# Optimization experiments

Measured on AMD Instinct MI355X. Metric: run time of the kernel, lower is better.

The kernel has to match this reference:

```python
import jax, jax.numpy as jnp
import numpy as np

# Model dims (match init_kwargs)
N_P, NV, P, S = 60, 5, 20, 14   # particles, vertices, pf features, sv features
HID, DE, DO, NCLS, BATCH = 60, 20, 24, 2, 512

# Rr/Rs one-hot matrices encode edges (r, s) for r != s with r varying slowest.
# So gather-by-Rr == repeat each node N-1 times, gather-by-Rs == index by senders,
# and scatter-sum by Rr^T == reshape to [B, N, N-1, De] and sum axis 2.
_SENDERS = np.array([s for r in range(N_P) for s in range(N_P) if s != r])


def _lin_params(key, din, dout):
    kw, kb = jax.random.split(key)
    bound = 1.0 / np.sqrt(din)
    w = jax.random.uniform(kw, (din, dout), minval=-bound, maxval=bound, dtype=jnp.float32)
    b = jax.random.uniform(kb, (dout,), minval=-bound, maxval=bound, dtype=jnp.float32)
    return w, b


def setup_inputs() -> dict:
    key = jax.random.key(0)
    ks = jax.random.split(key, 12)
    inp = {
        'x': jax.random.normal(ks[0], (BATCH, P, N_P), dtype=jnp.float32),
        'y': jax.random.normal(ks[1], (BATCH, S, NV), dtype=jnp.float32),
    }
    specs = [('fr', [(2 * P, HID), (HID, HID), (HID, DE)]),
             ('pv', [(S + P, HID), (HID, HID), (HID, DE)]),
             ('fo', [(P + 2 * DE, HID), (HID, HID), (HID, DO)])]
    ki = 2
    for name, dims in specs:
        for j, (di, do) in enumerate(dims, 1):
            w, b = _lin_params(ks[ki], di, do)
            ki += 1
            inp[f'{name}_w{j}'] = w
            inp[f'{name}_b{j}'] = b
    w, b = _lin_params(ks[11], DO, NCLS)
    inp['fc_w'] = w
    inp['fc_b'] = b
    return inp


def _mlp3(h, w1, b1, w2, b2, w3, b3):
    h = jax.nn.relu(h @ w1 + b1)
    h = jax.nn.relu(h @ w2 + b2)
    return jax.nn.relu(h @ w3 + b3)


def reference(x, y, fr_w1, fr_b1, fr_w2, fr_b2, fr_w3, fr_b3,
              pv_w1, pv_b1, pv_w2, pv_b2, pv_w3, pv_b3,
              fo_w1, fo_b1, fo_w2, fo_b2, fo_w3, fo_b3, fc_w, fc_b):
    xt = jnp.swapaxes(x, -1, -2)  # [B, N, P]
    yt = jnp.swapaxes(y, -1, -2)  # [B, Nv, S]
    B = xt.shape[0]

    # particle-particle edge conv (gather via index, scatter-sum via reshape)
    Orr = jnp.repeat(xt, N_P - 1, axis=1)          # [B, Nr, P], receiver features
    Ors = xt[:, _SENDERS]                          # [B, Nr, P], sender features
    E = _mlp3(jnp.concatenate([Orr, Ors], axis=-1),
              fr_w1, fr_b1, fr_w2, fr_b2, fr_w3, fr_b3)  # [B, Nr, De]
    Ebar_pp = E.reshape(B, N_P, N_P - 1, DE).sum(axis=2)  # [B, N, De]

    # particle-vertex edge conv (Rk repeats particles, Rv tiles vertices)
    Ork = jnp.repeat(xt, NV, axis=1)               # [B, Nt, P]
    Orv = jnp.tile(yt, (1, N_P, 1))                # [B, Nt, S]
    E2 = _mlp3(jnp.concatenate([Ork, Orv], axis=-1),
               pv_w1, pv_b1, pv_w2, pv_b2, pv_w3, pv_b3)  # [B, Nt, De]
    Ebar_pv = E2.reshape(B, N_P, NV, DE).sum(axis=2)      # [B, N, De]

    C = jnp.concatenate([xt, Ebar_pp, Ebar_pv], axis=-1)  # [B, N, P + 2*De]
    O = _mlp3(C, fo_w1, fo_b1, fo_w2, fo_b2, fo_w3, fo_b3)  # [B, N, Do]
    return O.sum(axis=-2) @ fc_w + fc_b  # [B, num_classes]
```

## Files before the change

kernel.cpp:

```cpp
#include <hip/hip_runtime.h>

#define BATCH 512
#define NPART 60
#define PFEAT 20
#define SFEAT 14
#define NVTX  5
#define HID   60
#define DE    20
#define DO    24
#define NCLS  2
#define SR    68

typedef _Float16 half8  __attribute__((ext_vector_type(8)));
typedef _Float16 half4v __attribute__((ext_vector_type(4)));
typedef __fp16   fp16x2 __attribute__((ext_vector_type(2)));
typedef float    f32x4  __attribute__((ext_vector_type(4)));

__device__ __forceinline__ half4v pkcvt4(f32x4 a) {
    fp16x2 lo = __builtin_amdgcn_cvt_pkrtz(a[0], a[1]);
    fp16x2 hi = __builtin_amdgcn_cvt_pkrtz(a[2], a[3]);
    half4v r;
    r[0] = (_Float16)lo[0]; r[1] = (_Float16)lo[1];
    r[2] = (_Float16)hi[0]; r[3] = (_Float16)hi[1];
    return r;
}
__device__ __forceinline__ half4v relu4(half4v a) {
#pragma unroll
    for (int j = 0; j < 4; ++j)
        a[j] = (a[j] > (_Float16)0.f) ? a[j] : (_Float16)0.f;
    return a;
}

__global__ __launch_bounds__(256) void prep_kernel(
    const float* __restrict__ x, const float* __restrict__ y,
    const float* __restrict__ fr_w1, const float* __restrict__ fr_b1,
    const float* __restrict__ pv_w1, const float* __restrict__ pv_b1,
    const float* __restrict__ fr_w2, const float* __restrict__ fr_b2,
    const float* __restrict__ fr_w3, const float* __restrict__ fr_b3,
    const float* __restrict__ pv_w2, const float* __restrict__ pv_b2,
    const float* __restrict__ pv_w3, const float* __restrict__ pv_b3,
    const float* __restrict__ fo_w1, const float* __restrict__ fo_b1,
    const float* __restrict__ fo_w2, const float* __restrict__ fo_b2,
    const float* __restrict__ fo_w3, const float* __restrict__ fo_b3,
    _Float16* __restrict__ frW2p, _Float16* __restrict__ frW3p16,
    _Float16* __restrict__ pvW2p, _Float16* __restrict__ pvW3p16,
    _Float16* __restrict__ foW1p, _Float16* __restrict__ foW2p16,
    _Float16* __restrict__ foW3p16,
    _Float16* __restrict__ frW1Ap, _Float16* __restrict__ frW1Bp,
    _Float16* __restrict__ pvW1Ap, _Float16* __restrict__ xp,
    _Float16* __restrict__ pvvp)
{
    if (blockIdx.x < 16) {
        int idx = blockIdx.x*256 + threadIdx.x;
        {
            int j  = idx & 7;
            int L  = (idx >> 3) & 63;
            int kk = (idx >> 9) & 1;
            int u  = idx >> 10;
            int k  = kk*32 + (L >> 4)*8 + j;
            int n  = u*16 + (L & 15);
            float v2f = 0.f, v2p = 0.f, v1o = 0.f;
            if (k < HID && n < HID) {
                v2f = fr_w2[k*HID + n];
                v2p = pv_w2[k*HID + n];
                v1o = fo_w1[k*HID + n];
            } else if (k == HID) {
                if (n < HID)      { v2f = fr_b2[n]; v2p = pv_b2[n]; v1o = fo_b1[n]; }
                else if (n == HID){ v2f = 1.f;      v2p = 1.f;      v1o = 1.f; }
            }
            frW2p[idx] = (_Float16)v2f;
            pvW2p[idx] = (_Float16)v2p;
            foW1p[idx] = (_Float16)v1o;
        }
        {
            int j  = idx & 3;
            int L  = (idx >> 2) & 63;
            int kt = (idx >> 8) & 3;
            int u  = idx >> 10;
            int k  = kt*16 + (L >> 4)*4 + j;
            int n  = u*16 + (L & 15);
            float v = 0.f;
            if (k < HID && n < HID)        v = fo_w2[k*HID + n];
            else if (k == HID) {
                if (n < HID)       v = fo_b2[n];
                else if (n == HID) v = 1.f;
            }
            foW2p16[idx] = (_Float16)v;
        }
        if (idx < 2048) {
            {
                int j  = idx & 3;
                int L  = (idx >> 2) & 63;
                int kt = (idx >> 8) & 3;
                int u  = idx >> 10;
                int k  = kt*16 + (L >> 4)*4 + j;
                int n  = u*16 + (L & 15);
                float vf = 0.f, vp = 0.f, vo = 0.f;
                if (k < HID) {
                    if (n < DE) { vf = fr_w3[k*DE + n]; vp = pv_w3[k*DE + n]; }
                    if (n < DO)   vo = fo_w3[k*DO + n];
                } else if (k == HID) {
                    if (n < DE) { vf = fr_b3[n]; vp = pv_b3[n]; }
                    if (n < DO)   vo = fo_b3[n];
                }
                frW3p16[idx] = (_Float16)vf;
                pvW3p16[idx] = (_Float16)vp;
                foW3p16[idx] = (_Float16)vo;
            }
            {
                int j = idx & 7;
                int L = (idx >> 3) & 63;
                int u = idx >> 9;
                int k = (L >> 4)*8 + j;
                int n = u*16 + (L & 15);
                float va = 0.f, vb = 0.f, vpv = 0.f;
                if (k < PFEAT && n < HID) {
                    va  = fr_w1[k*HID + n];
                    vb  = fr_w1[(PFEAT + k)*HID + n];
                    vpv = pv_w1[k*HID + n];
                } else if (k == PFEAT) {
                    if (n < HID)       va = fr_b1[n];
                    else if (n == HID) va = 1.f;
                }
                frW1Ap[idx] = (_Float16)va;
                frW1Bp[idx] = (_Float16)vb;
                pvW1Ap[idx] = (_Float16)vpv;
            }
        }
    } else if (blockIdx.x < 16 + 480) {
        int idx = (blockIdx.x - 16)*256 + threadIdx.x;
        if (idx < BATCH*NPART*4) {
            int p = idx % NPART;
            int t = idx / NPART;
            int q = t & 3;
            int b = t >> 2;
            half8 v;
#pragma unroll
            for (int j = 0; j < 8; ++j) {
                int k = q*8 + j;
                float f = 0.f;
                if (k < PFEAT)       f = x[((size_t)b*PFEAT + k)*NPART + p];
                else if (k == PFEAT) f = 1.f;
                v[j] = (_Float16)f;
            }
            *(half8*)(xp + (size_t)idx*8) = v;
        }
    } else {
        int idx = (blockIdx.x - (16 + 480))*256 + threadIdx.x;
        if (idx < BATCH*NVTX*64) {
            int h = idx & 63;
            int t = idx >> 6;
            int v = t % NVTX;
            int b = t / NVTX;
            float a;
            if (h < HID) {
                a = pv_b1[h];
#pragma unroll
                for (int f = 0; f < SFEAT; ++f)
                    a += y[((size_t)b*SFEAT + f)*NVTX + v] * pv_w1[(PFEAT + f)*HID + h];
            } else {
                a = (h == HID) ? 1.f : 0.f;
            }
            pvvp[idx] = (_Float16)a;
        }
    }
}

__global__ __launch_bounds__(512) void fused_kernel(
    const float* __restrict__ fcw, const float* __restrict__ fcb,
    const half8*  __restrict__ frw2p, const half4v* __restrict__ frw3p16,
    const half8*  __restrict__ pvw2p, const half4v* __restrict__ pvw3p16,
    const half8*  __restrict__ fow1p, const half4v* __restrict__ fow2p16,
    const half4v* __restrict__ fow3p16,
    const half8*  __restrict__ frw1ap, const half8* __restrict__ frw1bp,
    const half8*  __restrict__ pvw1ap, const _Float16* __restrict__ xp,
    const half8*  __restrict__ pvvp,
    float* __restrict__ out)
{
    __shared__ __align__(16) _Float16 sFrA[NPART*SR];
    __shared__ __align__(16) _Float16 sFrB[NPART*SR];
    __shared__ __align__(16) _Float16 sPvA[NPART*SR];
    __shared__ __align__(16) _Float16 sEpp[NPART*DE];
    __shared__ __align__(16) _Float16 sEpvP[NVTX*NPART*DE];
    __shared__ __align__(16) float    sDsum[4][DO];
    _Float16* sCin = sFrA;

    const f32x4 z4 = {0.f, 0.f, 0.f, 0.f};

    int bb   = blockIdx.x;
    int wv   = threadIdx.x >> 6;
    int lane = threadIdx.x & 63;
    int ml   = lane & 15;
    int q    = lane >> 4;

    half4v onesA;
#pragma unroll
    for (int j = 0; j < 4; ++j) onesA[j] = (_Float16)1.f;

    {
        int tile = wv & 3;
        int row  = 16*tile + ml;
        int rr   = (row < NPART) ? row : 0;
        half8 bX = *(const half8*)(xp + (((size_t)bb*4 + q)*NPART + rr)*8);
#pragma unroll
        for (int task = 0; task < 2; ++task) {
            const half8* Wt; _Float16* Ot;
            if (wv < 4) {
                if (task == 0) { Wt = frw1ap; Ot = sFrA; }
                else           { Wt = pvw1ap; Ot = sPvA; }
            } else {
                if (task == 1) break;
                Wt = frw1bp; Ot = sFrB;
            }
#pragma unroll
            for (int u = 0; u < 4; ++u) {
                half8 w8 = Wt[u*64 + lane];
                f32x4 acc = z4;
                acc = __builtin_amdgcn_mfma_f32_16x16x32_f16(w8, bX, acc, 0, 0, 0);
                if (row < NPART)
                    *(half4v*)(Ot + row*SR + u*16 + 4*q) = pkcvt4(acc);
            }
        }
    }
    __syncthreads();

    {
        half8  w2r[8];
        half4v w3r[8];
#pragma unroll
        for (int t = 0; t < 8; ++t) w2r[t] = frw2p[t*64 + lane];
#pragma unroll
        for (int t = 0; t < 8; ++t) w3r[t] = frw3p16[t*64 + lane];
#pragma unroll
        for (int t = 0; t < 8; ++t) {
            asm volatile("" : "+v"(w2r[t]));
            asm volatile("" : "+v"(w3r[t]));
        }
        half4v m3;
#pragma unroll
        for (int j = 0; j < 4; ++j) m3[j] = (_Float16)((4*q + j < 11) ? 1.f : 0.f);

        for (int r = wv; r < NPART; r += 8) {
            half8 u8k0 = *(const half8*)(sFrA + r*SR + q*8);
            half8 u8k1 = *(const half8*)(sFrA + r*SR + 32 + q*8);
            f32x4 accS0 = z4, accS1 = z4;

#pragma unroll
            for (int c = 0; c < 4; ++c) {
                int edge = 16*c + ml;
                int sr = (edge < NPART-1) ? (edge + (edge >= r)) : 0;
                half8 bA0, bA1;
                {
                    half8 v8 = *(const half8*)(sFrB + sr*SR + q*8);
                    half8 s8 = u8k0 + v8;
#pragma unroll
                    for (int j = 0; j < 8; ++j)
                        s8[j] = (s8[j] > (_Float16)0.f) ? s8[j] : (_Float16)0.f;
                    bA0 = s8;
                    v8 = *(const half8*)(sFrB + sr*SR + 32 + q*8);
                    s8 = u8k1 + v8;
#pragma unroll
                    for (int j = 0; j < 8; ++j)
                        s8[j] = (s8[j] > (_Float16)0.f) ? s8[j] : (_Float16)0.f;
                    bA1 = s8;
                }
                half4v a3u[4];
#pragma unroll
                for (int u = 0; u < 4; ++u) {
                    f32x4 a = z4;
                    a = __builtin_amdgcn_mfma_f32_16x16x32_f16(w2r[u*2 + 0], bA0, a, 0, 0, 0);
                    a = __builtin_amdgcn_mfma_f32_16x16x32_f16(w2r[u*2 + 1], bA1, a, 0, 0, 0);
                    a3u[u] = relu4(pkcvt4(a));
                }
                f32x4 e0 = z4, e1 = z4;
#pragma unroll
                for (int u = 0; u < 4; ++u) {
                    e0 = __builtin_amdgcn_mfma_f32_16x16x16f16(a3u[u], w3r[0*4 + u], e0, 0, 0, 0);
                    e1 = __builtin_amdgcn_mfma_f32_16x16x16f16(a3u[u], w3r[1*4 + u], e1, 0, 0, 0);
                }
                half4v p0 = relu4(pkcvt4(e0));
                half4v p1 = relu4(pkcvt4(e1));
                if (c == 3) { p0 *= m3; p1 *= m3; }
                accS0 = __builtin_amdgcn_mfma_f32_16x16x16f16(onesA, p0, accS0, 0, 0, 0);
                accS1 = __builtin_amdgcn_mfma_f32_16x16x16f16(onesA, p1, accS1, 0, 0, 0);
            }
            if (q == 0) {
                sEpp[r*DE + ml] = (_Float16)accS0[0];
                if (ml < DE - 16)
                    sEpp[r*DE + 16 + ml] = (_Float16)accS1[0];
            }
        }
    }

    if (wv >= 4) {
        half8  w2r[8];
        half4v w3r[8];
#pragma unroll
        for (int t = 0; t < 8; ++t) w2r[t] = pvw2p[t*64 + lane];
#pragma unroll
        for (int t = 0; t < 8; ++t) w3r[t] = pvw3p16[t*64 + lane];
#pragma unroll
        for (int t = 0; t < 8; ++t) {
            asm volatile("" : "+v"(w2r[t]));
            asm volatile("" : "+v"(w3r[t]));
        }
        for (int kunit = wv - 4; kunit < 20; kunit += 4) {
            int gv = kunit >> 2;
            int tl = kunit & 3;
            int p  = 16*tl + ml;
            int sp = (p < NPART) ? p : 0;
            const half8* pvvB = pvvp + ((size_t)bb*NVTX + gv)*8;
            half8 u8k0 = pvvB[q];
            half8 u8k1 = pvvB[4 + q];

            half8 bA[2];
#pragma unroll
            for (int kk = 0; kk < 2; ++kk) {
                half8 v8 = *(const half8*)(sPvA + sp*SR + kk*32 + q*8);
                half8 s8 = (kk ? u8k1 : u8k0) + v8;
#pragma unroll
                for (int j = 0; j < 8; ++j) {
                    _Float16 vj = s8[j];
                    s8[j] = (vj > (_Float16)0.f) ? vj : (_Float16)0.f;
                }
                bA[kk] = s8;
            }
            f32x4 acc3[2];
            acc3[0] = z4; acc3[1] = z4;
#pragma unroll
            for (int u = 0; u < 4; ++u) {
                f32x4 a = z4;
                a = __builtin_amdgcn_mfma_f32_16x16x32_f16(w2r[u*2 + 0], bA[0], a, 0, 0, 0);
                a = __builtin_amdgcn_mfma_f32_16x16x32_f16(w2r[u*2 + 1], bA[1], a, 0, 0, 0);
                half4v a3u = relu4(pkcvt4(a));
                acc3[0] = __builtin_amdgcn_mfma_f32_16x16x16f16(w3r[0*4 + u], a3u, acc3[0], 0, 0, 0);
                acc3[1] = __builtin_amdgcn_mfma_f32_16x16x16f16(w3r[1*4 + u], a3u, acc3[1], 0, 0, 0);
            }
#pragma unroll
            for (int v = 0; v < 2; ++v) {
                int col4 = v*16 + 4*q;
                if (p < NPART && col4 < DE) {
                    half4v hv = relu4(pkcvt4(acc3[v]));
                    *(half4v*)(sEpvP + (gv*NPART + p)*DE + col4) = hv;
                }
            }
        }
    }
    __syncthreads();

    for (int idx = threadIdx.x; idx < NPART*64; idx += 512) {
        int p = idx >> 6;
        int k = idx & 63;
        _Float16 v;
        if (k < PFEAT) {
            v = xp[(((size_t)bb*4 + (k >> 3))*NPART + p)*8 + (k & 7)];
        } else if (k < PFEAT + DE) {
            v = sEpp[p*DE + (k - PFEAT)];
        } else if (k < PFEAT + 2*DE) {
            int c = k - PFEAT - DE;
            float s = 0.f;
#pragma unroll
            for (int g5 = 0; g5 < NVTX; ++g5)
                s += (float)sEpvP[(g5*NPART + p)*DE + c];
            v = (_Float16)s;
        } else {
            v = (k == HID) ? (_Float16)1.f : (_Float16)0.f;
        }
        sCin[p*SR + k] = v;
    }
    __syncthreads();

    if (wv < 4) {
        int p = 16*wv + ml;
        int sp = (p < NPART) ? p : 0;
        half8 bC[2];
#pragma unroll
        for (int kk = 0; kk < 2; ++kk)
            bC[kk] = *(const half8*)(sCin + sp*SR + kk*32 + q*8);

        f32x4 acc1[4];
#pragma unroll
        for (int u = 0; u < 4; ++u) {
            acc1[u] = z4;
            acc1[u] = __builtin_amdgcn_mfma_f32_16x16x32_f16(fow1p[(u*2 + 0)*64 + lane], bC[0], acc1[u], 0, 0, 0);
            acc1[u] = __builtin_amdgcn_mfma_f32_16x16x32_f16(fow1p[(u*2 + 1)*64 + lane], bC[1], acc1[u], 0, 0, 0);
        }
        half4v a2[4];
#pragma unroll
        for (int u = 0; u < 4; ++u) a2[u] = relu4(pkcvt4(acc1[u]));

        f32x4 acc2[4];
#pragma unroll
        for (int u = 0; u < 4; ++u) {
            acc2[u] = z4;
#pragma unroll
            for (int kt = 0; kt < 4; ++kt)
                acc2[u] = __builtin_amdgcn_mfma_f32_16x16x16f16(fow2p16[(u*4 + kt)*64 + lane], a2[kt], acc2[u], 0, 0, 0);
        }
        half4v a3[4];
#pragma unroll
        for (int u = 0; u < 4; ++u) a3[u] = relu4(pkcvt4(acc2[u]));

        f32x4 e0 = z4, e1 = z4;
#pragma unroll
        for (int u = 0; u < 4; ++u) {
            e0 = __builtin_amdgcn_mfma_f32_16x16x16f16(a3[u], fow3p16[(0*4 + u)*64 + lane], e0, 0, 0, 0);
            e1 = __builtin_amdgcn_mfma_f32_16x16x16f16(a3[u], fow3p16[(1*4 + u)*64 + lane], e1, 0, 0, 0);
        }
        half4v p0 = relu4(pkcvt4(e0));
        half4v p1 = relu4(pkcvt4(e1));
        if (wv == 3 && q == 3) {
#pragma unroll
            for (int j = 0; j < 4; ++j) { p0[j] = (_Float16)0.f; p1[j] = (_Float16)0.f; }
        }
        f32x4 accP0 = __builtin_amdgcn_mfma_f32_16x16x16f16(onesA, p0, z4, 0, 0, 0);
        f32x4 accP1 = __builtin_amdgcn_mfma_f32_16x16x16f16(onesA, p1, z4, 0, 0, 0);
        if (q == 0) {
            sDsum[wv][ml] = accP0[0];
            if (ml < DO - 16)
                sDsum[wv][16 + ml] = accP1[0];
        }
    }
    __syncthreads();

    if (wv == 0) {
        float tot = 0.f;
        if (lane < DO) {
#pragma unroll
            for (int w4 = 0; w4 < 4; ++w4) tot += sDsum[w4][lane];
        }
        float p0 = (lane < DO) ? tot * fcw[lane*NCLS + 0] : 0.f;
        float p1 = (lane < DO) ? tot * fcw[lane*NCLS + 1] : 0.f;
#pragma unroll
        for (int d = 1; d <= 16; d <<= 1) {
            p0 += __shfl_xor(p0, d);
            p1 += __shfl_xor(p1, d);
        }
        if (lane == 0) {
            out[bb*NCLS + 0] = p0 + fcb[0];
            out[bb*NCLS + 1] = p1 + fcb[1];
        }
    }
}

extern "C" void kernel_launch(void* const* d_in, const int* in_sizes, int n_in,
                              void* d_out, int out_size, void* d_ws, size_t ws_size,
                              hipStream_t stream)
{
    const float* x     = (const float*)d_in[0];
    const float* y     = (const float*)d_in[1];
    const float* fr_w1 = (const float*)d_in[2];
    const float* fr_b1 = (const float*)d_in[3];
    const float* fr_w2 = (const float*)d_in[4];
    const float* fr_b2 = (const float*)d_in[5];
    const float* fr_w3 = (const float*)d_in[6];
    const float* fr_b3 = (const float*)d_in[7];
    const float* pv_w1 = (const float*)d_in[8];
    const float* pv_b1 = (const float*)d_in[9];
    const float* pv_w2 = (const float*)d_in[10];
    const float* pv_b2 = (const float*)d_in[11];
    const float* pv_w3 = (const float*)d_in[12];
    const float* pv_b3 = (const float*)d_in[13];
    const float* fo_w1 = (const float*)d_in[14];
    const float* fo_b1 = (const float*)d_in[15];
    const float* fo_w2 = (const float*)d_in[16];
    const float* fo_b2 = (const float*)d_in[17];
    const float* fo_w3 = (const float*)d_in[18];
    const float* fo_b3 = (const float*)d_in[19];
    const float* fc_w  = (const float*)d_in[20];
    const float* fc_b  = (const float*)d_in[21];
    float* out = (float*)d_out;

    char* wsb = (char*)d_ws;
    size_t off = 0;
    auto alloc = [&](size_t bytes) { char* p = wsb + off; off += (bytes + 255) & ~(size_t)255; return p; };

    _Float16* frW2p   = (_Float16*)alloc(4096*2);
    _Float16* frW3p16 = (_Float16*)alloc(2048*2);
    _Float16* pvW2p   = (_Float16*)alloc(4096*2);
    _Float16* pvW3p16 = (_Float16*)alloc(2048*2);
    _Float16* foW1p   = (_Float16*)alloc(4096*2);
    _Float16* foW2p16 = (_Float16*)alloc(4096*2);
    _Float16* foW3p16 = (_Float16*)alloc(2048*2);
    _Float16* frW1Ap  = (_Float16*)alloc(2048*2);
    _Float16* frW1Bp  = (_Float16*)alloc(2048*2);
    _Float16* pvW1Ap  = (_Float16*)alloc(2048*2);
    _Float16* xp      = (_Float16*)alloc((size_t)BATCH*NPART*32*2);
    _Float16* pvvp    = (_Float16*)alloc((size_t)BATCH*NVTX*64*2);

    int xblocks  = (BATCH*NPART*4 + 255)/256;
    int pvblocks = (BATCH*NVTX*64 + 255)/256;
    prep_kernel<<<16 + xblocks + pvblocks, 256, 0, stream>>>(
        x, y, fr_w1, fr_b1, pv_w1, pv_b1,
        fr_w2, fr_b2, fr_w3, fr_b3,
        pv_w2, pv_b2, pv_w3, pv_b3,
        fo_w1, fo_b1, fo_w2, fo_b2, fo_w3, fo_b3,
        frW2p, frW3p16, pvW2p, pvW3p16, foW1p, foW2p16, foW3p16,
        frW1Ap, frW1Bp, pvW1Ap, xp, pvvp);

    fused_kernel<<<BATCH, 512, 0, stream>>>(
        fc_w, fc_b,
        (const half8*)frW2p, (const half4v*)frW3p16,
        (const half8*)pvW2p, (const half4v*)pvW3p16,
        (const half8*)foW1p, (const half4v*)foW2p16, (const half4v*)foW3p16,
        (const half8*)frW1Ap, (const half8*)frW1Bp,
        (const half8*)pvW1Ap, xp, (const half8*)pvvp,
        out);
}
```

Before: 134.4 us.

## Use 16x16x32 MFMA for layer 2/3, sentinel padding row, register-accumulate PV edges

Repacks the second- and third-layer weights so the K=64 products run as two 16x16x32 f16 MFMAs instead of four 16x16x16 ones. Adds a sentinel sender row set to a large negative value, so padded edges go through ReLU to zero without a per-tile mask multiply. The particle-vertex path now has each wave own one particle tile, loop over vertices and accumulate the ReLU outputs in registers. This removes the 5x staging buffer in shared memory and the later summation pass. Particle-particle sums are written straight into the C-input buffer, which drops the sEpp copy and reduces LDS use, with the risk that the repacked weight layouts must exactly match the MFMA operand layout.

```diff
diff --git a/kernel.cpp b/kernel.cpp
--- a/kernel.cpp
+++ b/kernel.cpp
@@ -29,6 +29,21 @@
     for (int j = 0; j < 4; ++j)
         a[j] = (a[j] > (_Float16)0.f) ? a[j] : (_Float16)0.f;
     return a;
+}
+__device__ __forceinline__ half8 cvtrelu8(f32x4 a, f32x4 b) {
+    fp16x2 c0 = __builtin_amdgcn_cvt_pkrtz(a[0], a[1]);
+    fp16x2 c1 = __builtin_amdgcn_cvt_pkrtz(a[2], a[3]);
+    fp16x2 c2 = __builtin_amdgcn_cvt_pkrtz(b[0], b[1]);
+    fp16x2 c3 = __builtin_amdgcn_cvt_pkrtz(b[2], b[3]);
+    half8 r;
+    r[0] = (_Float16)c0[0]; r[1] = (_Float16)c0[1];
+    r[2] = (_Float16)c1[0]; r[3] = (_Float16)c1[1];
+    r[4] = (_Float16)c2[0]; r[5] = (_Float16)c2[1];
+    r[6] = (_Float16)c3[0]; r[7] = (_Float16)c3[1];
+#pragma unroll
+    for (int j = 0; j < 8; ++j)
+        r[j] = (r[j] > (_Float16)0.f) ? r[j] : (_Float16)0.f;
+    return r;
 }
 
 __global__ __launch_bounds__(256) void prep_kernel(
@@ -42,10 +57,10 @@
     const float* __restrict__ fo_w1, const float* __restrict__ fo_b1,
     const float* __restrict__ fo_w2, const float* __restrict__ fo_b2,
     const float* __restrict__ fo_w3, const float* __restrict__ fo_b3,
-    _Float16* __restrict__ frW2p, _Float16* __restrict__ frW3p16,
-    _Float16* __restrict__ pvW2p, _Float16* __restrict__ pvW3p16,
-    _Float16* __restrict__ foW1p, _Float16* __restrict__ foW2p16,
-    _Float16* __restrict__ foW3p16,
+    _Float16* __restrict__ frW2p, _Float16* __restrict__ frW3x,
+    _Float16* __restrict__ pvW2p, _Float16* __restrict__ pvW3x,
+    _Float16* __restrict__ foW1p, _Float16* __restrict__ foW2x,
+    _Float16* __restrict__ foW3x,
     _Float16* __restrict__ frW1Ap, _Float16* __restrict__ frW1Bp,
     _Float16* __restrict__ pvW1Ap, _Float16* __restrict__ xp,
     _Float16* __restrict__ pvvp)
@@ -73,28 +88,30 @@
             foW1p[idx] = (_Float16)v1o;
         }
         {
-            int j  = idx & 3;
-            int L  = (idx >> 2) & 63;
-            int kt = (idx >> 8) & 3;
-            int u  = idx >> 10;
-            int k  = kt*16 + (L >> 4)*4 + j;
-            int n  = u*16 + (L & 15);
+            int j    = idx & 7;
+            int L    = (idx >> 3) & 63;
+            int pair = (idx >> 9) & 1;
+            int u    = idx >> 10;
+            int qq   = L >> 4;
+            int k    = pair*32 + ((j < 4) ? (qq*4 + j) : (16 + qq*4 + (j - 4)));
+            int n    = u*16 + (L & 15);
             float v = 0.f;
-            if (k < HID && n < HID)        v = fo_w2[k*HID + n];
+            if (k < HID) { if (n < HID) v = fo_w2[k*HID + n]; }
             else if (k == HID) {
                 if (n < HID)       v = fo_b2[n];
                 else if (n == HID) v = 1.f;
             }
-            foW2p16[idx] = (_Float16)v;
+            foW2x[idx] = (_Float16)v;
         }
         if (idx < 2048) {
             {
-                int j  = idx & 3;
-                int L  = (idx >> 2) & 63;
-                int kt = (idx >> 8) & 3;
-                int u  = idx >> 10;
-                int k  = kt*16 + (L >> 4)*4 + j;
-                int n  = u*16 + (L & 15);
+                int j    = idx & 7;
+                int L    = (idx >> 3) & 63;
+                int pair = (idx >> 9) & 1;
+                int v2   = idx >> 10;
+                int qq   = L >> 4;
+                int k    = pair*32 + ((j < 4) ? (qq*4 + j) : (16 + qq*4 + (j - 4)));
+                int n    = v2*16 + (L & 15);
                 float vf = 0.f, vp = 0.f, vo = 0.f;
                 if (k < HID) {
                     if (n < DE) { vf = fr_w3[k*DE + n]; vp = pv_w3[k*DE + n]; }
@@ -103,9 +120,9 @@
                     if (n < DE) { vf = fr_b3[n]; vp = pv_b3[n]; }
                     if (n < DO)   vo = fo_b3[n];
                 }
-                frW3p16[idx] = (_Float16)vf;
-                pvW3p16[idx] = (_Float16)vp;
-                foW3p16[idx] = (_Float16)vo;
+                frW3x[idx] = (_Float16)vf;
+                pvW3x[idx] = (_Float16)vp;
+                foW3x[idx] = (_Float16)vo;
             }
             {
                 int j = idx & 7;
@@ -168,20 +185,19 @@
 
 __global__ __launch_bounds__(512) void fused_kernel(
     const float* __restrict__ fcw, const float* __restrict__ fcb,
-    const half8*  __restrict__ frw2p, const half4v* __restrict__ frw3p16,
-    const half8*  __restrict__ pvw2p, const half4v* __restrict__ pvw3p16,
-    const half8*  __restrict__ fow1p, const half4v* __restrict__ fow2p16,
-    const half4v* __restrict__ fow3p16,
+    const half8*  __restrict__ frw2p, const half8* __restrict__ frw3x,
+    const half8*  __restrict__ pvw2p, const half8* __restrict__ pvw3x,
+    const half8*  __restrict__ fow1p, const half8* __restrict__ fow2x,
+    const half8*  __restrict__ fow3x,
     const half8*  __restrict__ frw1ap, const half8* __restrict__ frw1bp,
     const half8*  __restrict__ pvw1ap, const _Float16* __restrict__ xp,
     const half8*  __restrict__ pvvp,
     float* __restrict__ out)
 {
     __shared__ __align__(16) _Float16 sFrA[NPART*SR];
-    __shared__ __align__(16) _Float16 sFrB[NPART*SR];
+    __shared__ __align__(16) _Float16 sFrB[64*SR];
     __shared__ __align__(16) _Float16 sPvA[NPART*SR];
-    __shared__ __align__(16) _Float16 sEpp[NPART*DE];
-    __shared__ __align__(16) _Float16 sEpvP[NVTX*NPART*DE];
+    __shared__ __align__(16) _Float16 sEpvP[NPART*DE];
     __shared__ __align__(16) float    sDsum[4][DO];
     _Float16* sCin = sFrA;
 
@@ -221,24 +237,24 @@
                     *(half4v*)(Ot + row*SR + u*16 + 4*q) = pkcvt4(acc);
             }
         }
+        if (threadIdx.x >= 256) {
+            int t = threadIdx.x - 256;
+            sFrB[(60 + (t >> 6))*SR + (t & 63)] = (_Float16)(-30000.f);
+        }
     }
     __syncthreads();
 
     {
-        half8  w2r[8];
-        half4v w3r[8];
+        half8 w2r[8];
+        half8 w3x[4];
 #pragma unroll
         for (int t = 0; t < 8; ++t) w2r[t] = frw2p[t*64 + lane];
 #pragma unroll
-        for (int t = 0; t < 8; ++t) w3r[t] = frw3p16[t*64 + lane];
-#pragma unroll
-        for (int t = 0; t < 8; ++t) {
-            asm volatile("" : "+v"(w2r[t]));
-            asm volatile("" : "+v"(w3r[t]));
-        }
-        half4v m3;
-#pragma unroll
-        for (int j = 0; j < 4; ++j) m3[j] = (_Float16)((4*q + j < 11) ? 1.f : 0.f);
+        for (int t = 0; t < 4; ++t) w3x[t] = frw3x[t*64 + lane];
+#pragma unroll
+        for (int t = 0; t < 8; ++t) asm volatile("" : "+v"(w2r[t]));
+#pragma unroll
+        for (int t = 0; t < 4; ++t) asm volatile("" : "+v"(w3x[t]));
 
         for (int r = wv; r < NPART; r += 8) {
             half8 u8k0 = *(const half8*)(sFrA + r*SR + q*8);
@@ -248,7 +264,7 @@
 #pragma unroll
             for (int c = 0; c < 4; ++c) {
                 int edge = 16*c + ml;
-                int sr = (edge < NPART-1) ? (edge + (edge >= r)) : 0;
+                int sr = (edge < NPART-1) ? (edge + (edge >= r)) : 60;
                 half8 bA0, bA1;
                 {
                     half8 v8 = *(const half8*)(sFrB + sr*SR + q*8);
@@ -264,86 +280,96 @@
                         s8[j] = (s8[j] > (_Float16)0.f) ? s8[j] : (_Float16)0.f;
                     bA1 = s8;
                 }
-                half4v a3u[4];
-#pragma unroll
-                for (int u = 0; u < 4; ++u) {
-                    f32x4 a = z4;
-                    a = __builtin_amdgcn_mfma_f32_16x16x32_f16(w2r[u*2 + 0], bA0, a, 0, 0, 0);
-                    a = __builtin_amdgcn_mfma_f32_16x16x32_f16(w2r[u*2 + 1], bA1, a, 0, 0, 0);
-                    a3u[u] = relu4(pkcvt4(a));
-                }
+                f32x4 L0 = z4, L1 = z4, L2 = z4, L3 = z4;
+                L0 = __builtin_amdgcn_mfma_f32_16x16x32_f16(w2r[0], bA0, L0, 0, 0, 0);
+                L0 = __builtin_amdgcn_mfma_f32_16x16x32_f16(w2r[1], bA1, L0, 0, 0, 0);
+                L1 = __builtin_amdgcn_mfma_f32_16x16x32_f16(w2r[2], bA0, L1, 0, 0, 0);
+                L1 = __builtin_amdgcn_mfma_f32_16x16x32_f16(w2r[3], bA1, L1, 0, 0, 0);
+                L2 = __builtin_amdgcn_mfma_f32_16x16x32_f16(w2r[4], bA0, L2, 0, 0, 0);
+                L2 = __builtin_amdgcn_mfma_f32_16x16x32_f16(w2r[5], bA1, L2, 0, 0, 0);
+                L3 = __builtin_amdgcn_mfma_f32_16x16x32_f16(w2r[6], bA0, L3, 0, 0, 0);
+                L3 = __builtin_amdgcn_mfma_f32_16x16x32_f16(w2r[7], bA1, L3, 0, 0, 0);
+                half8 a3p0 = cvtrelu8(L0, L1);
+                half8 a3p1 = cvtrelu8(L2, L3);
                 f32x4 e0 = z4, e1 = z4;
-#pragma unroll
-                for (int u = 0; u < 4; ++u) {
-                    e0 = __builtin_amdgcn_mfma_f32_16x16x16f16(a3u[u], w3r[0*4 + u], e0, 0, 0, 0);
-                    e1 = __builtin_amdgcn_mfma_f32_16x16x16f16(a3u[u], w3r[1*4 + u], e1, 0, 0, 0);
-                }
+                e0 = __builtin_amdgcn_mfma_f32_16x16x32_f16(a3p0, w3x[0], e0, 0, 0, 0);
+                e0 = __builtin_amdgcn_mfma_f32_16x16x32_f16(a3p1, w3x[1], e0, 0, 0, 0);
+                e1 = __builtin_amdgcn_mfma_f32_16x16x32_f16(a3p0, w3x[2], e1, 0, 0, 0);
+                e1 = __builtin_amdgcn_mfma_f32_16x16x32_f16(a3p1, w3x[3], e1, 0, 0, 0);
                 half4v p0 = relu4(pkcvt4(e0));
                 half4v p1 = relu4(pkcvt4(e1));
-                if (c == 3) { p0 *= m3; p1 *= m3; }
                 accS0 = __builtin_amdgcn_mfma_f32_16x16x16f16(onesA, p0, accS0, 0, 0, 0);
                 accS1 = __builtin_amdgcn_mfma_f32_16x16x16f16(onesA, p1, accS1, 0, 0, 0);
             }
             if (q == 0) {
-                sEpp[r*DE + ml] = (_Float16)accS0[0];
+                sCin[r*SR + PFEAT + ml] = (_Float16)accS0[0];
                 if (ml < DE - 16)
-                    sEpp[r*DE + 16 + ml] = (_Float16)accS1[0];
+                    sCin[r*SR + PFEAT + 16 + ml] = (_Float16)accS1[0];
             }
         }
     }
 
     if (wv >= 4) {
-        half8  w2r[8];
-        half4v w3r[8];
+        int tl = wv - 4;
+        int p  = 16*tl + ml;
+        int sp = (p < NPART) ? p : 0;
+        half8 w2r[8];
+        half8 w3x[4];
 #pragma unroll
         for (int t = 0; t < 8; ++t) w2r[t] = pvw2p[t*64 + lane];
 #pragma unroll
-        for (int t = 0; t < 8; ++t) w3r[t] = pvw3p16[t*64 + lane];
-#pragma unroll
-        for (int t = 0; t < 8; ++t) {
-            asm volatile("" : "+v"(w2r[t]));
-            asm volatile("" : "+v"(w3r[t]));
-        }
-        for (int kunit = wv - 4; kunit < 20; kunit += 4) {
-            int gv = kunit >> 2;
-            int tl = kunit & 3;
-            int p  = 16*tl + ml;
-            int sp = (p < NPART) ? p : 0;
+        for (int t = 0; t < 4; ++t) w3x[t] = pvw3x[t*64 + lane];
+#pragma unroll
+        for (int t = 0; t < 8; ++t) asm volatile("" : "+v"(w2r[t]));
+#pragma unroll
+        for (int t = 0; t < 4; ++t) asm volatile("" : "+v"(w3x[t]));
+
+        f32x4 accf0 = z4, accf1 = z4;
+        for (int gv = 0; gv < NVTX; ++gv) {
             const half8* pvvB = pvvp + ((size_t)bb*NVTX + gv)*8;
             half8 u8k0 = pvvB[q];
             half8 u8k1 = pvvB[4 + q];
-
-            half8 bA[2];
-#pragma unroll
-            for (int kk = 0; kk < 2; ++kk) {
-                half8 v8 = *(const half8*)(sPvA + sp*SR + kk*32 + q*8);
-                half8 s8 = (kk ? u8k1 : u8k0) + v8;
-#pragma unroll
-                for (int j = 0; j < 8; ++j) {
-                    _Float16 vj = s8[j];
-                    s8[j] = (vj > (_Float16)0.f) ? vj : (_Float16)0.f;
-                }
-                bA[kk] = s8;
-            }
-            f32x4 acc3[2];
-            acc3[0] = z4; acc3[1] = z4;
-#pragma unroll
-            for (int u = 0; u < 4; ++u) {
-                f32x4 a = z4;
-                a = __builtin_amdgcn_mfma_f32_16x16x32_f16(w2r[u*2 + 0], bA[0], a, 0, 0, 0);
-                a = __builtin_amdgcn_mfma_f32_16x16x32_f16(w2r[u*2 + 1], bA[1], a, 0, 0, 0);
-                half4v a3u = relu4(pkcvt4(a));
-                acc3[0] = __builtin_amdgcn_mfma_f32_16x16x16f16(w3r[0*4 + u], a3u, acc3[0], 0, 0, 0);
-                acc3[1] = __builtin_amdgcn_mfma_f32_16x16x16f16(w3r[1*4 + u], a3u, acc3[1], 0, 0, 0);
-            }
-#pragma unroll
-            for (int v = 0; v < 2; ++v) {
-                int col4 = v*16 + 4*q;
-                if (p < NPART && col4 < DE) {
-                    half4v hv = relu4(pkcvt4(acc3[v]));
-                    *(half4v*)(sEpvP + (gv*NPART + p)*DE + col4) = hv;
-                }
-            }
+            half8 bA0, bA1;
+            {
+                half8 v8 = *(const half8*)(sPvA + sp*SR + q*8);
+                half8 s8 = u8k0 + v8;
+#pragma unroll
+                for (int j = 0; j < 8; ++j)
+                    s8[j] = (s8[j] > (_Float16)0.f) ? s8[j] : (_Float16)0.f;
+                bA0 = s8;
+                v8 = *(const half8*)(sPvA + sp*SR + 32 + q*8);
+                s8 = u8k1 + v8;
+#pragma unroll
+                for (int j = 0; j < 8; ++j)
+                    s8[j] = (s8[j] > (_Float16)0.f) ? s8[j] : (_Float16)0.f;
+                bA1 = s8;
+            }
+            f32x4 L0 = z4, L1 = z4, L2 = z4, L3 = z4;
+            L0 = __builtin_amdgcn_mfma_f32_16x16x32_f16(w2r[0], bA0, L0, 0, 0, 0);
+            L0 = __builtin_amdgcn_mfma_f32_16x16x32_f16(w2r[1], bA1, L0, 0, 0, 0);
+            L1 = __builtin_amdgcn_mfma_f32_16x16x32_f16(w2r[2], bA0, L1, 0, 0, 0);
+            L1 = __builtin_amdgcn_mfma_f32_16x16x32_f16(w2r[3], bA1, L1, 0, 0, 0);
+            L2 = __builtin_amdgcn_mfma_f32_16x16x32_f16(w2r[4], bA0, L2, 0, 0, 0);
+            L2 = __builtin_amdgcn_mfma_f32_16x16x32_f16(w2r[5], bA1, L2, 0, 0, 0);
+            L3 = __builtin_amdgcn_mfma_f32_16x16x32_f16(w2r[6], bA0, L3, 0, 0, 0);
+            L3 = __builtin_amdgcn_mfma_f32_16x16x32_f16(w2r[7], bA1, L3, 0, 0, 0);
+            half8 a3p0 = cvtrelu8(L0, L1);
+            half8 a3p1 = cvtrelu8(L2, L3);
+            f32x4 a30 = z4, a31 = z4;
+            a30 = __builtin_amdgcn_mfma_f32_16x16x32_f16(w3x[0], a3p0, a30, 0, 0, 0);
+            a30 = __builtin_amdgcn_mfma_f32_16x16x32_f16(w3x[1], a3p1, a30, 0, 0, 0);
+            a31 = __builtin_amdgcn_mfma_f32_16x16x32_f16(w3x[2], a3p0, a31, 0, 0, 0);
+            a31 = __builtin_amdgcn_mfma_f32_16x16x32_f16(w3x[3], a3p1, a31, 0, 0, 0);
+#pragma unroll
+            for (int i = 0; i < 4; ++i) {
+                accf0[i] += fmaxf(a30[i], 0.f);
+                accf1[i] += fmaxf(a31[i], 0.f);
+            }
+        }
+        if (p < NPART) {
+            *(half4v*)(sEpvP + p*DE + 4*q) = pkcvt4(accf0);
+            if (q == 0)
+                *(half4v*)(sEpvP + p*DE + 16) = pkcvt4(accf1);
         }
     }
     __syncthreads();
@@ -351,18 +377,12 @@
     for (int idx = threadIdx.x; idx < NPART*64; idx += 512) {
         int p = idx >> 6;
         int k = idx & 63;
+        if (k >= PFEAT && k < PFEAT + DE) continue;
         _Float16 v;
         if (k < PFEAT) {
             v = xp[(((size_t)bb*4 + (k >> 3))*NPART + p)*8 + (k & 7)];
-        } else if (k < PFEAT + DE) {
-            v = sEpp[p*DE + (k - PFEAT)];
         } else if (k < PFEAT + 2*DE) {
-            int c = k - PFEAT - DE;
-            float s = 0.f;
-#pragma unroll
-            for (int g5 = 0; g5 < NVTX; ++g5)
-                s += (float)sEpvP[(g5*NPART + p)*DE + c];
-            v = (_Float16)s;
+            v = sEpvP[p*DE + (k - PFEAT - DE)];
         } else {
             v = (k == HID) ? (_Float16)1.f : (_Float16)0.f;
         }
@@ -385,28 +405,24 @@
             acc1[u] = __builtin_amdgcn_mfma_f32_16x16x32_f16(fow1p[(u*2 + 0)*64 + lane], bC[0], acc1[u], 0, 0, 0);
             acc1[u] = __builtin_amdgcn_mfma_f32_16x16x32_f16(fow1p[(u*2 + 1)*64 + lane], bC[1], acc1[u], 0, 0, 0);
         }
-        half4v a2[4];
-#pragma unroll
-        for (int u = 0; u < 4; ++u) a2[u] = relu4(pkcvt4(acc1[u]));
+        half8 a2p0 = cvtrelu8(acc1[0], acc1[1]);
+        half8 a2p1 = cvtrelu8(acc1[2], acc1[3]);
 
         f32x4 acc2[4];
 #pragma unroll
         for (int u = 0; u < 4; ++u) {
             acc2[u] = z4;
-#pragma unroll
-            for (int kt = 0; kt < 4; ++kt)
-                acc2[u] = __builtin_amdgcn_mfma_f32_16x16x16f16(fow2p16[(u*4 + kt)*64 + lane], a2[kt], acc2[u], 0, 0, 0);
-        }
-        half4v a3[4];
-#pragma unroll
-        for (int u = 0; u < 4; ++u) a3[u] = relu4(pkcvt4(acc2[u]));
+            acc2[u] = __builtin_amdgcn_mfma_f32_16x16x32_f16(fow2x[(u*2 + 0)*64 + lane], a2p0, acc2[u], 0, 0, 0);
+            acc2[u] = __builtin_amdgcn_mfma_f32_16x16x32_f16(fow2x[(u*2 + 1)*64 + lane], a2p1, acc2[u], 0, 0, 0);
+        }
+        half8 a3p0 = cvtrelu8(acc2[0], acc2[1]);
+        half8 a3p1 = cvtrelu8(acc2[2], acc2[3]);
 
         f32x4 e0 = z4, e1 = z4;
-#pragma unroll
-        for (int u = 0; u < 4; ++u) {
-            e0 = __builtin_amdgcn_mfma_f32_16x16x16f16(a3[u], fow3p16[(0*4 + u)*64 + lane], e0, 0, 0, 0);
-            e1 = __builtin_amdgcn_mfma_f32_16x16x16f16(a3[u], fow3p16[(1*4 + u)*64 + lane], e1, 0, 0, 0);
-        }
+        e0 = __builtin_amdgcn_mfma_f32_16x16x32_f16(a3p0, fow3x[0*64 + lane], e0, 0, 0, 0);
+        e0 = __builtin_amdgcn_mfma_f32_16x16x32_f16(a3p1, fow3x[1*64 + lane], e0, 0, 0, 0);
+        e1 = __builtin_amdgcn_mfma_f32_16x16x32_f16(a3p0, fow3x[2*64 + lane], e1, 0, 0, 0);
+        e1 = __builtin_amdgcn_mfma_f32_16x16x32_f16(a3p1, fow3x[3*64 + lane], e1, 0, 0, 0);
         half4v p0 = relu4(pkcvt4(e0));
         half4v p1 = relu4(pkcvt4(e1));
         if (wv == 3 && q == 3) {
@@ -476,12 +492,12 @@
     auto alloc = [&](size_t bytes) { char* p = wsb + off; off += (bytes + 255) & ~(size_t)255; return p; };
 
     _Float16* frW2p   = (_Float16*)alloc(4096*2);
-    _Float16* frW3p16 = (_Float16*)alloc(2048*2);
+    _Float16* frW3x   = (_Float16*)alloc(2048*2);
     _Float16* pvW2p   = (_Float16*)alloc(4096*2);
-    _Float16* pvW3p16 = (_Float16*)alloc(2048*2);
+    _Float16* pvW3x   = (_Float16*)alloc(2048*2);
     _Float16* foW1p   = (_Float16*)alloc(4096*2);
-    _Float16* foW2p16 = (_Float16*)alloc(4096*2);
-    _Float16* foW3p16 = (_Float16*)alloc(2048*2);
+    _Float16* foW2x   = (_Float16*)alloc(4096*2);
+    _Float16* foW3x   = (_Float16*)alloc(2048*2);
     _Float16* frW1Ap  = (_Float16*)alloc(2048*2);
     _Float16* frW1Bp  = (_Float16*)alloc(2048*2);
     _Float16* pvW1Ap  = (_Float16*)alloc(2048*2);
@@ -495,14 +511,14 @@
         fr_w2, fr_b2, fr_w3, fr_b3,
         pv_w2, pv_b2, pv_w3, pv_b3,
         fo_w1, fo_b1, fo_w2, fo_b2, fo_w3, fo_b3,
-        frW2p, frW3p16, pvW2p, pvW3p16, foW1p, foW2p16, foW3p16,
+        frW2p, frW3x, pvW2p, pvW3x, foW1p, foW2x, foW3x,
         frW1Ap, frW1Bp, pvW1Ap, xp, pvvp);
 
     fused_kernel<<<BATCH, 512, 0, stream>>>(
         fc_w, fc_b,
-        (const half8*)frW2p, (const half4v*)frW3p16,
-        (const half8*)pvW2p, (const half4v*)pvW3p16,
-        (const half8*)foW1p, (const half4v*)foW2p16, (const half4v*)foW3p16,
+        (const half8*)frW2p, (const half8*)frW3x,
+        (const half8*)pvW2p, (const half8*)pvW3x,
+        (const half8*)foW1p, (const half8*)foW2x, (const half8*)foW3x,
         (const half8*)frW1Ap, (const half8*)frW1Bp,
         (const half8*)pvW1Ap, xp, (const half8*)pvvp,
         out);
```

New measurement: 129.1 us. 4.0% less time.
